# Kernel tuning notes

Hardware: AMD Instinct MI355X
Metric: run time of the kernel (lower is better)

## Reference

```python
import jax, jax.numpy as jnp
import numpy as np

EPS = 1e-6
K = 20
B, N = 4, 4096
HID, CDIM = 128, 64


def vn_lin(W, x):
    # W: [Cout, Cin], x: [B, Cin, 3, ...] -> [B, Cout, 3, ...]
    return jnp.einsum('oc,bc...->bo...', W, x)


def vn_leaky(x, d, ns=0.0):
    # vector-neuron leaky ReLU: reflect the part of x anti-aligned with direction d
    dot = jnp.sum(x * d, axis=2, keepdims=True)
    dsq = jnp.sum(d * d, axis=2, keepdims=True)
    return ns * x + (1.0 - ns) * jnp.where(dot >= 0, x, x - (dot / (dsq + EPS)) * d)


def vn_max_pool(x, Wd):
    # pool over the LAST axis, picking per-(b,c) the vector maximizing <x, d>
    d = vn_lin(Wd, x)
    dot = jnp.sum(x * d, axis=2, keepdims=True)            # [B,C,1,...,L]
    idx = jnp.broadcast_to(jnp.argmax(dot, axis=-1), x.shape[:-1])
    return jnp.take_along_axis(x, idx[..., None], axis=-1)[..., 0]


def graph_feature_cross(pts, k):
    # pts: [B, N, 3] -> [B, 3ch, 3vec, N, k] with channels (nbr-x, x, cross(nbr,x))
    sq = jnp.sum(pts * pts, axis=-1)
    inner = jnp.einsum('bnd,bmd->bnm', pts, pts)
    neg_dist = 2.0 * inner - sq[:, :, None] - sq[:, None, :]
    _, idx = jax.lax.top_k(neg_dist, k)                     # [B, N, k]
    nbr = jax.vmap(lambda p, i: p[i])(pts, idx)             # [B, N, k, 3]
    x = jnp.broadcast_to(pts[:, :, None, :], nbr.shape)
    cross = jnp.cross(nbr, x, axis=-1)
    feat = jnp.stack([nbr - x, x, cross], axis=3)           # [B, N, k, 3ch, 3vec]
    return jnp.transpose(feat, (0, 3, 4, 1, 2))


def resblock(x, a0, f0, a1, f1, sc):
    net = vn_lin(f0, vn_leaky(x, vn_lin(a0, x)))
    dx = vn_lin(f1, vn_leaky(net, vn_lin(a1, net)))
    return vn_lin(sc, x) + dx


def _init(key, shape, fan_in):
    return jax.random.normal(key, shape, jnp.float32) / np.sqrt(fan_in)


def setup_inputs():
    key = jax.random.key(0)
    ks = jax.random.split(key, 14)
    return {
        'pc': jax.random.normal(ks[0], (B, N, 3), jnp.float32),
        'conv_Wf': _init(ks[1], (64, 3), 3),
        'conv_Wd': _init(ks[2], (64, 3), 3),
        'pool_pos_Wd': _init(ks[3], (64, 64), 64),
        'fc_pos_W': _init(ks[4], (2 * HID, 64), 64),
        'blk_a0': _init(ks[5], (5, 2 * HID, 2 * HID), 2 * HID),
        'blk_f0': _init(ks[6], (5, HID, 2 * HID), 2 * HID),
        'blk_a1': _init(ks[7], (5, HID, HID), HID),
        'blk_f1': _init(ks[8], (5, HID, HID), HID),
        'blk_sc': _init(ks[9], (5, HID, 2 * HID), 2 * HID),
        'pool_Wd': _init(ks[10], (5, HID, HID), HID),
        'actc_Wd': _init(ks[11], (HID, HID), HID),
        'fcc_W': _init(ks[12], (CDIM, HID), HID),
    }


def reference(pc, conv_Wf, conv_Wd, pool_pos_Wd, fc_pos_W, blk_a0, blk_f0, blk_a1, blk_f1, blk_sc, pool_Wd, actc_Wd, fcc_W):
    b = pc.shape[0]
    feat = graph_feature_cross(pc, K)                         # [B,3,3,N,k]
    net = vn_leaky(vn_lin(conv_Wf, feat), vn_lin(conv_Wd, feat))  # [B,64,3,N,k]
    net = vn_max_pool(net, pool_pos_Wd)                       # [B,64,3,N] (pool over k)
    net = vn_lin(fc_pos_W, net)                               # [B,256,3,N]
    for i in range(5):
        net = resblock(net, blk_a0[i], blk_f0[i], blk_a1[i], blk_f1[i], blk_sc[i])  # [B,128,3,N]
        if i < 4:
            pooled = vn_max_pool(net, pool_Wd[i])             # [B,128,3] (pool over N)
            net = jnp.concatenate([net, jnp.broadcast_to(pooled[..., None], net.shape)], axis=1)
    net = vn_max_pool(net, pool_Wd[4])                        # [B,128,3]
    c = vn_lin(fcc_W, vn_leaky(net, vn_lin(actc_Wd, net)))    # [B,64,3]
    return c.reshape(b, -1)                                   # [B,192]
```

## Files before the change

### kernel.cpp

```cpp
#include <hip/hip_runtime.h>
#include <hip/hip_bf16.h>
#include <math.h>

#define NPTS 4096
#define NB 4
#define KNN 20
#define NCOLS (3*NPTS)
#define NEG_INF (-__builtin_huge_valf())
#define DNEG_INF (-__builtin_huge_val())

typedef _Float16 f16x8 __attribute__((ext_vector_type(8)));
typedef _Float16 f16x4 __attribute__((ext_vector_type(4)));
typedef float f32x4 __attribute__((ext_vector_type(4)));

#define WOFF_FC 0
#define WOFF_A0 16384
#define WOFF_F0 344064
#define WOFF_A1 507904
#define WOFF_F1 589824
#define WOFF_SC 671744
#define WOFF_PW 835584
#define WTOT    917504

__global__ __launch_bounds__(512) void knn_kernel(const float* __restrict__ pc,
                                                  int* __restrict__ idx) {
  __shared__ float pts[NPTS*3];
  __shared__ double msv[2][8];
  __shared__ int    msn[2][8];
  int b = blockIdx.x >> 10;
  int rowblk = blockIdx.x & 1023;
  const float* pb = pc + (size_t)b*NPTS*3;
  for (int i = threadIdx.x; i < NPTS*3; i += 512) pts[i] = pb[i];
  __syncthreads();
  int wave = threadIdx.x >> 6;
  int lane = threadIdx.x & 63;
  int row  = wave >> 1;
  int half = wave & 1;
  int l128 = half*64 + lane;
  int n = rowblk*4 + row;
  double pn0 = pts[n*3+0], pn1 = pts[n*3+1], pn2 = pts[n*3+2];
  double sqn = pn0*pn0 + pn1*pn1 + pn2*pn2;
  double nd[32];
#pragma unroll
  for (int j = 0; j < 32; ++j) {
    int m = j*128 + l128;
    double q0 = pts[m*3+0], q1 = pts[m*3+1], q2 = pts[m*3+2];
    double inner = pn0*q0 + pn1*q1 + pn2*q2;
    double sqm = q0*q0 + q1*q1 + q2*q2;
    nd[j] = 2.0*inner - sqn - sqm;
  }
  double gm[2]; int gj[2];
#pragma unroll
  for (int g = 0; g < 2; ++g) {
    double v = nd[g*16]; int jb = g*16;
#pragma unroll
    for (int jj = 1; jj < 16; ++jj) {
      int j = g*16 + jj;
      bool take = nd[j] > v;
      v = take ? nd[j] : v;
      jb = take ? j : jb;
    }
    gm[g] = v; gj[g] = jb;
  }
  int* orow = idx + ((size_t)b*NPTS + n)*KNN;
  for (int t = 0; t < KNN; ++t) {
    double bv = gm[0]; int bj = gj[0];
    if (gm[1] > bv) { bv = gm[1]; bj = gj[1]; }
    int bm = bj*128 + l128;
#pragma unroll
    for (int s = 1; s < 64; s <<= 1) {
      double ov = __shfl_xor(bv, s, 64);
      int om = __shfl_xor(bm, s, 64);
      bool take = (ov > bv) || (ov == bv && om < bm);
      bv = take ? ov : bv;
      bm = take ? om : bm;
    }
    if (lane == 0) { msv[t&1][wave] = bv; msn[t&1][wave] = bm; }
    __syncthreads();
    {
      double pv = msv[t&1][wave^1]; int pm = msn[t&1][wave^1];
      bool take = (pv > bv) || (pv == bv && pm < bm);
      bv = take ? pv : bv;
      bm = take ? pm : bm;
    }
    if (half == 0 && lane == 0) orow[t] = bm;
    if (t < KNN-1) {
      int vic_l128 = bm & 127;
      int jw = bm >> 7;
      int vic_half = vic_l128 >> 6;
      if (vic_half == half) {
        bool iswl = (l128 == vic_l128);
        int gw = jw >> 4;
#define REBUILD(G) { \
  _Pragma("unroll") \
  for (int jj = 0; jj < 16; ++jj) { \
    int j = (G)*16 + jj; \
    if (iswl && j == jw) nd[j] = DNEG_INF; \
  } \
  double v = nd[(G)*16]; int jb = (G)*16; \
  _Pragma("unroll") \
  for (int jj = 1; jj < 16; ++jj) { \
    int j = (G)*16 + jj; \
    bool take = nd[j] > v; \
    v = take ? nd[j] : v; \
    jb = take ? j : jb; \
  } \
  gm[G] = v; gj[G] = jb; \
}
        if (gw == 0) REBUILD(0)
        else         REBUILD(1)
#undef REBUILD
      }
    }
  }
}

#define ECH 5
__global__ __launch_bounds__(128) void edgeconv_kernel(
    const float* __restrict__ pc, const int* __restrict__ knnidx,
    const float* __restrict__ Wf, const float* __restrict__ Wd,
    const float* __restrict__ Wp, float* __restrict__ outp) {
  __shared__ float xls[2*ECH*3*64];
  int wave = threadIdx.x >> 6, lane = threadIdx.x & 63;
  int pid0 = blockIdx.x * 2;
  int b = pid0 >> 12;
  int n = (pid0 & (NPTS-1)) + wave;
  const float* pb = pc + (size_t)b*NPTS*3;
  int c = lane;
  float wrow[64];
#pragma unroll
  for (int j = 0; j < 64; ++j) wrow[j] = Wp[c*64 + j];
  float wf0 = Wf[c*3+0], wf1 = Wf[c*3+1], wf2 = Wf[c*3+2];
  float wd0 = Wd[c*3+0], wd1 = Wd[c*3+1], wd2 = Wd[c*3+2];
  float f9[9];
#pragma unroll
  for (int i = 0; i < 9; ++i) f9[i] = 0.0f;
  if (lane < KNN) {
    int j = knnidx[((size_t)b*NPTS + n)*KNN + lane];
    float q0 = pb[j*3+0], q1 = pb[j*3+1], q2 = pb[j*3+2];
    float x0 = pb[n*3+0], x1 = pb[n*3+1], x2 = pb[n*3+2];
    f9[0] = q0-x0; f9[1] = q1-x1; f9[2] = q2-x2;
    f9[3] = x0;    f9[4] = x1;    f9[5] = x2;
    f9[6] = q1*x2 - q2*x1;
    f9[7] = q2*x0 - q0*x2;
    f9[8] = q0*x1 - q1*x0;
  }
  float* xw = &xls[wave*ECH*3*64];
  double bdot = DNEG_INF;
  float bx0 = 0.f, bx1 = 0.f, bx2 = 0.f;
  for (int k0 = 0; k0 < KNN; k0 += ECH) {
    for (int kc = 0; kc < ECH; ++kc) {
      int kk = k0 + kc;
      float fch[9];
#pragma unroll
      for (int i = 0; i < 9; ++i) fch[i] = __shfl(f9[i], kk, 64);
      float fv[3], dv[3];
#pragma unroll
      for (int v = 0; v < 3; ++v) {
        fv[v] = wf0*fch[v] + wf1*fch[3+v] + wf2*fch[6+v];
        dv[v] = wd0*fch[v] + wd1*fch[3+v] + wd2*fch[6+v];
      }
      float dot = fv[0]*dv[0] + fv[1]*dv[1] + fv[2]*dv[2];
      if (dot < 0.0f) {
        float dsq = dv[0]*dv[0] + dv[1]*dv[1] + dv[2]*dv[2];
        float s = dot / (dsq + 1e-6f);
        fv[0] -= s*dv[0]; fv[1] -= s*dv[1]; fv[2] -= s*dv[2];
      }
      xw[(0*ECH+kc)*64 + c] = fv[0];
      xw[(1*ECH+kc)*64 + c] = fv[1];
      xw[(2*ECH+kc)*64 + c] = fv[2];
    }
    for (int kc = 0; kc < ECH; ++kc) {
      float a0 = 0.f, a1 = 0.f, a2 = 0.f;
#pragma unroll
      for (int j = 0; j < 64; j += 4) {
        float4 v0 = *(const float4*)&xw[(0*ECH+kc)*64 + j];
        float4 v1 = *(const float4*)&xw[(1*ECH+kc)*64 + j];
        float4 v2 = *(const float4*)&xw[(2*ECH+kc)*64 + j];
        a0 += wrow[j]*v0.x + wrow[j+1]*v0.y + wrow[j+2]*v0.z + wrow[j+3]*v0.w;
        a1 += wrow[j]*v1.x + wrow[j+1]*v1.y + wrow[j+2]*v1.z + wrow[j+3]*v1.w;
        a2 += wrow[j]*v2.x + wrow[j+1]*v2.y + wrow[j+2]*v2.z + wrow[j+3]*v2.w;
      }
      float xc0 = xw[(0*ECH+kc)*64 + c];
      float xc1 = xw[(1*ECH+kc)*64 + c];
      float xc2 = xw[(2*ECH+kc)*64 + c];
      double dd = (double)xc0*a0 + (double)xc1*a1 + (double)xc2*a2;
      bool take = dd > bdot;
      bdot = take ? dd : bdot;
      bx0 = take ? xc0 : bx0;
      bx1 = take ? xc1 : bx1;
      bx2 = take ? xc2 : bx2;
    }
  }
  outp[((size_t)b*NCOLS + 0*NPTS + n)*64 + c] = bx0;
  outp[((size_t)b*NCOLS + 1*NPTS + n)*64 + c] = bx1;
  outp[((size_t)b*NCOLS + 2*NPTS + n)*64 + c] = bx2;
}

__global__ __launch_bounds__(256) void wsplit_kernel(
    const float* __restrict__ fc, const float* __restrict__ a0,
    const float* __restrict__ f0, const float* __restrict__ a1,
    const float* __restrict__ f1, const float* __restrict__ sc,
    const float* __restrict__ pw, _Float16* __restrict__ outp) {
  int i = blockIdx.x*256 + threadIdx.x;
  const float* src; int off;
  if      (i < WOFF_A0) { src = fc; off = WOFF_FC; }
  else if (i < WOFF_F0) { src = a0; off = WOFF_A0; }
  else if (i < WOFF_A1) { src = f0; off = WOFF_F0; }
  else if (i < WOFF_F1) { src = a1; off = WOFF_A1; }
  else if (i < WOFF_SC) { src = f1; off = WOFF_F1; }
  else if (i < WOFF_PW) { src = sc; off = WOFF_SC; }
  else                  { src = pw; off = WOFF_PW; }
  float w = src[i - off];
  _Float16 h = (_Float16)w;
  outp[i] = h;
  outp[i + WTOT] = (_Float16)(w - (float)h);
}

__global__ __launch_bounds__(256) void bias2_kernel(
    const float* __restrict__ Wa0, const float* __restrict__ Wsc,
    const float* __restrict__ pooled,
    float* __restrict__ biasA, float* __restrict__ biasS) {
  int id = blockIdx.x*256 + threadIdx.x;
  const float* W; float* dst; int Cout; int idx;
  if (id < NB*3*256) { W = Wa0; dst = biasA; Cout = 256; idx = id; }
  else               { W = Wsc; dst = biasS; Cout = 128; idx = id - NB*3*256; }
  int co = idx % Cout; int t = idx / Cout;
  int v = t % 3; int b = t / 3;
  double acc = 0.0;
  const float* wr = W + (size_t)co*256 + 128;
  const float* pp = pooled + (size_t)b*384 + v;
#pragma unroll 4
  for (int c = 0; c < 128; ++c)
    acc += (double)wr[c] * (double)pp[c*3];
  dst[idx] = (float)acc;
}

#define LDP 40
__global__ __launch_bounds__(256) void gemm_mfma(
    const _Float16* __restrict__ Wh, const _Float16* __restrict__ Wl,
    const float* __restrict__ X, const float* __restrict__ Z,
    const float* __restrict__ bias, float* __restrict__ Y,
    int Cin, int Wstride, int ldX, int ldY, int ldZ, int addZ, int Cbias) {
  __shared__ __align__(16) _Float16 Ah[64*LDP];
  __shared__ __align__(16) _Float16 Al[64*LDP];
  __shared__ __align__(16) _Float16 Bh[128*LDP];
  __shared__ __align__(16) _Float16 Bl[128*LDP];
  int b = blockIdx.z;
  int sp0 = blockIdx.x * 64;
  int co0 = blockIdx.y * 128;
  const float* Xb = X + ((size_t)b*NCOLS + sp0) * ldX;
  int t = threadIdx.x;
  int arow = t >> 2, akoff = (t & 3) * 8;
  int brow = t >> 1, bkoff = (t & 1) * 16;
  int wid = t >> 6, lane = t & 63;
  int wr = (wid >> 1) * 32, wc = (wid & 1) * 64;
  int lrow = lane & 15, lk = (lane >> 4) * 8;
  f32x4 acc[2][4];
#pragma unroll
  for (int f = 0; f < 2; ++f)
#pragma unroll
    for (int g = 0; g < 4; ++g)
#pragma unroll
      for (int r = 0; r < 4; ++r) acc[f][g][r] = 0.0f;

  for (int k0 = 0; k0 < Cin; k0 += 32) {
    const float* xs = Xb + (size_t)arow*ldX + k0 + akoff;
    float xv[8];
    *(float4*)&xv[0] = *(const float4*)&xs[0];
    *(float4*)&xv[4] = *(const float4*)&xs[4];
    _Float16 xh[8], xl[8];
#pragma unroll
    for (int j = 0; j < 8; ++j) {
      _Float16 h = (_Float16)xv[j];
      xh[j] = h; xl[j] = (_Float16)(xv[j] - (float)h);
    }
    *(f16x8*)&Ah[arow*LDP + akoff] = *(f16x8*)&xh[0];
    *(f16x8*)&Al[arow*LDP + akoff] = *(f16x8*)&xl[0];
    const _Float16* whs = Wh + (size_t)(co0 + brow)*Wstride + k0 + bkoff;
    const _Float16* wls = Wl + (size_t)(co0 + brow)*Wstride + k0 + bkoff;
    *(f16x8*)&Bh[brow*LDP + bkoff]     = *(const f16x8*)&whs[0];
    *(f16x8*)&Bh[brow*LDP + bkoff + 8] = *(const f16x8*)&whs[8];
    *(f16x8*)&Bl[brow*LDP + bkoff]     = *(const f16x8*)&wls[0];
    *(f16x8*)&Bl[brow*LDP + bkoff + 8] = *(const f16x8*)&wls[8];
    __syncthreads();
    f16x8 ah[2], al[2], bh[4], bl[4];
#pragma unroll
    for (int f = 0; f < 2; ++f) {
      ah[f] = *(f16x8*)&Ah[(wr + f*16 + lrow)*LDP + lk];
      al[f] = *(f16x8*)&Al[(wr + f*16 + lrow)*LDP + lk];
    }
#pragma unroll
    for (int g = 0; g < 4; ++g) {
      bh[g] = *(f16x8*)&Bh[(wc + g*16 + lrow)*LDP + lk];
      bl[g] = *(f16x8*)&Bl[(wc + g*16 + lrow)*LDP + lk];
    }
#pragma unroll
    for (int f = 0; f < 2; ++f)
#pragma unroll
      for (int g = 0; g < 4; ++g) {
        acc[f][g] = __builtin_amdgcn_mfma_f32_16x16x32_f16(ah[f], bh[g], acc[f][g], 0, 0, 0);
        acc[f][g] = __builtin_amdgcn_mfma_f32_16x16x32_f16(ah[f], bl[g], acc[f][g], 0, 0, 0);
        acc[f][g] = __builtin_amdgcn_mfma_f32_16x16x32_f16(al[f], bh[g], acc[f][g], 0, 0, 0);
      }
    __syncthreads();
  }
  int lr0 = (lane >> 4) * 4, lc = lane & 15;
  float badd[4] = {0.f, 0.f, 0.f, 0.f};
  if (bias) {
    int v = sp0 >> 12;
    const float* brow2 = bias + ((size_t)b*3 + v)*Cbias;
#pragma unroll
    for (int g = 0; g < 4; ++g) badd[g] = brow2[co0 + wc + g*16 + lc];
  }
#pragma unroll
  for (int f = 0; f < 2; ++f)
#pragma unroll
    for (int g = 0; g < 4; ++g)
#pragma unroll
      for (int r = 0; r < 4; ++r) {
        int sp = sp0 + wr + f*16 + lr0 + r;
        int co = co0 + wc + g*16 + lc;
        float val = acc[f][g][r] + badd[g];
        if (addZ) val += Z[((size_t)b*NCOLS + sp)*ldZ + co];
        Y[((size_t)b*NCOLS + sp)*ldY + co] = val;
      }
}

__global__ __launch_bounds__(256) void gemm_dual(
    const _Float16* __restrict__ W1h, const _Float16* __restrict__ W1l,
    const _Float16* __restrict__ W2h, const _Float16* __restrict__ W2l,
    const float* __restrict__ X1, const float* __restrict__ X2s,
    const float* __restrict__ bias, float* __restrict__ Y,
    int K2, int ldY, int Cbias) {
  __shared__ __align__(16) _Float16 Ah[64*LDP];
  __shared__ __align__(16) _Float16 Al[64*LDP];
  __shared__ __align__(16) _Float16 Bh[128*LDP];
  __shared__ __align__(16) _Float16 Bl[128*LDP];
  int b = blockIdx.z;
  int sp0 = blockIdx.x * 64;
  int co0 = blockIdx.y * 128;
  int t = threadIdx.x;
  int arow = t >> 2, akoff = (t & 3) * 8;
  int brow = t >> 1, bkoff = (t & 1) * 16;
  int wid = t >> 6, lane = t & 63;
  int wr = (wid >> 1) * 32, wc = (wid & 1) * 64;
  int lrow = lane & 15, lk = (lane >> 4) * 8;
  f32x4 acc[2][4];
#pragma unroll
  for (int f = 0; f < 2; ++f)
#pragma unroll
    for (int g = 0; g < 4; ++g)
#pragma unroll
      for (int r = 0; r < 4; ++r) acc[f][g][r] = 0.0f;

  int Ktot = 128 + K2;
  for (int k0 = 0; k0 < Ktot; k0 += 32) {
    const float* xs;
    const _Float16 *whs, *wls;
    if (k0 < 128) {
      xs  = X1 + ((size_t)b*NCOLS + sp0 + arow)*128 + k0 + akoff;
      whs = W1h + (size_t)(co0 + brow)*128 + k0 + bkoff;
      wls = W1l + (size_t)(co0 + brow)*128 + k0 + bkoff;
    } else {
      xs  = X2s + ((size_t)b*NCOLS + sp0 + arow)*256 + (k0-128) + akoff;
      whs = W2h + (size_t)(co0 + brow)*256 + (k0-128) + bkoff;
      wls = W2l + (size_t)(co0 + brow)*256 + (k0-128) + bkoff;
    }
    float xv[8];
    *(float4*)&xv[0] = *(const float4*)&xs[0];
    *(float4*)&xv[4] = *(const float4*)&xs[4];
    _Float16 xh[8], xl[8];
#pragma unroll
    for (int j = 0; j < 8; ++j) {
      _Float16 h = (_Float16)xv[j];
      xh[j] = h; xl[j] = (_Float16)(xv[j] - (float)h);
    }
    *(f16x8*)&Ah[arow*LDP + akoff] = *(f16x8*)&xh[0];
    *(f16x8*)&Al[arow*LDP + akoff] = *(f16x8*)&xl[0];
    *(f16x8*)&Bh[brow*LDP + bkoff]     = *(const f16x8*)&whs[0];
    *(f16x8*)&Bh[brow*LDP + bkoff + 8] = *(const f16x8*)&whs[8];
    *(f16x8*)&Bl[brow*LDP + bkoff]     = *(const f16x8*)&wls[0];
    *(f16x8*)&Bl[brow*LDP + bkoff + 8] = *(const f16x8*)&wls[8];
    __syncthreads();
    f16x8 ah[2], al[2], bh[4], bl[4];
#pragma unroll
    for (int f = 0; f < 2; ++f) {
      ah[f] = *(f16x8*)&Ah[(wr + f*16 + lrow)*LDP + lk];
      al[f] = *(f16x8*)&Al[(wr + f*16 + lrow)*LDP + lk];
    }
#pragma unroll
    for (int g = 0; g < 4; ++g) {
      bh[g] = *(f16x8*)&Bh[(wc + g*16 + lrow)*LDP + lk];
      bl[g] = *(f16x8*)&Bl[(wc + g*16 + lrow)*LDP + lk];
    }
#pragma unroll
    for (int f = 0; f < 2; ++f)
#pragma unroll
      for (int g = 0; g < 4; ++g) {
        acc[f][g] = __builtin_amdgcn_mfma_f32_16x16x32_f16(ah[f], bh[g], acc[f][g], 0, 0, 0);
        acc[f][g] = __builtin_amdgcn_mfma_f32_16x16x32_f16(ah[f], bl[g], acc[f][g], 0, 0, 0);
        acc[f][g] = __builtin_amdgcn_mfma_f32_16x16x32_f16(al[f], bh[g], acc[f][g], 0, 0, 0);
      }
    __syncthreads();
  }
  int lr0 = (lane >> 4) * 4, lc = lane & 15;
  float badd[4] = {0.f, 0.f, 0.f, 0.f};
  if (bias) {
    int v = sp0 >> 12;
    const float* brow2 = bias + ((size_t)b*3 + v)*Cbias;
#pragma unroll
    for (int g = 0; g < 4; ++g) badd[g] = brow2[co0 + wc + g*16 + lc];
  }
#pragma unroll
  for (int f = 0; f < 2; ++f)
#pragma unroll
    for (int g = 0; g < 4; ++g)
#pragma unroll
      for (int r = 0; r < 4; ++r) {
        int sp = sp0 + wr + f*16 + lr0 + r;
        int co = co0 + wc + g*16 + lc;
        Y[((size_t)b*NCOLS + sp)*ldY + co] = acc[f][g][r] + badd[g];
      }
}

template<int FM>
__global__ __launch_bounds__(256) void gemm_leaky(
    const _Float16* __restrict__ Wh, const _Float16* __restrict__ Wl,
    const float* __restrict__ X, const float* __restrict__ pooled,
    const float* __restrict__ bias, float* __restrict__ Y,
    int Cin, int Wstride, int ldX, int ldY, int Cbias) {
  constexpr int BM = FM*32;
  __shared__ __align__(16) _Float16 Ah[BM*LDP];
  __shared__ __align__(16) _Float16 Al[BM*LDP];
  __shared__ __align__(16) _Float16 Bh[128*LDP];
  __shared__ __align__(16) _Float16 Bl[128*LDP];
  int b = blockIdx.z;
  int n0 = blockIdx.x * BM;
  int co0 = blockIdx.y * 128;
  int t = threadIdx.x;
  constexpr int APT = BM/8;
  constexpr int TPR = 32/APT;
  int arow = t / TPR, akoff = (t % TPR) * APT;
  int brow = t >> 1, bkoff = (t & 1) * 16;
  int wid = t >> 6, lane = t & 63;
  int wr = (wid >> 1) * (BM/2), wc = (wid & 1) * 64;
  int lrow = lane & 15, lk = (lane >> 4) * 8;
  f32x4 acc[3][FM][4];
#pragma unroll
  for (int v = 0; v < 3; ++v)
#pragma unroll
    for (int f = 0; f < FM; ++f)
#pragma unroll
      for (int g = 0; g < 4; ++g)
#pragma unroll
        for (int r = 0; r < 4; ++r) acc[v][f][g][r] = 0.0f;

  for (int v = 0; v < 3; ++v) {
    const float* Xb = X + ((size_t)b*NCOLS + (size_t)v*NPTS + n0) * ldX;
    for (int k0 = 0; k0 < Cin; k0 += 32) {
      const float* xs = Xb + (size_t)arow*ldX + k0 + akoff;
      float xv[APT];
#pragma unroll
      for (int j = 0; j < APT; j += 4)
        *(float4*)&xv[j] = *(const float4*)&xs[j];
      _Float16 xh[APT], xl[APT];
#pragma unroll
      for (int j = 0; j < APT; ++j) {
        _Float16 h = (_Float16)xv[j];
        xh[j] = h; xl[j] = (_Float16)(xv[j] - (float)h);
      }
      if (APT == 8) {
        *(f16x8*)&Ah[arow*LDP + akoff] = *(f16x8*)&xh[0];
        *(f16x8*)&Al[arow*LDP + akoff] = *(f16x8*)&xl[0];
      } else {
        *(f16x4*)&Ah[arow*LDP + akoff] = *(f16x4*)&xh[0];
        *(f16x4*)&Al[arow*LDP + akoff] = *(f16x4*)&xl[0];
      }
      const _Float16* whs = Wh + (size_t)(co0 + brow)*Wstride + k0 + bkoff;
      const _Float16* wls = Wl + (size_t)(co0 + brow)*Wstride + k0 + bkoff;
      *(f16x8*)&Bh[brow*LDP + bkoff]     = *(const f16x8*)&whs[0];
      *(f16x8*)&Bh[brow*LDP + bkoff + 8] = *(const f16x8*)&whs[8];
      *(f16x8*)&Bl[brow*LDP + bkoff]     = *(const f16x8*)&wls[0];
      *(f16x8*)&Bl[brow*LDP + bkoff + 8] = *(const f16x8*)&wls[8];
      __syncthreads();
      f16x8 ah[FM], al[FM], bh[4], bl[4];
#pragma unroll
      for (int f = 0; f < FM; ++f) {
        ah[f] = *(f16x8*)&Ah[(wr + f*16 + lrow)*LDP + lk];
        al[f] = *(f16x8*)&Al[(wr + f*16 + lrow)*LDP + lk];
      }
#pragma unroll
      for (int g = 0; g < 4; ++g) {
        bh[g] = *(f16x8*)&Bh[(wc + g*16 + lrow)*LDP + lk];
        bl[g] = *(f16x8*)&Bl[(wc + g*16 + lrow)*LDP + lk];
      }
#pragma unroll
      for (int f = 0; f < FM; ++f)
#pragma unroll
        for (int g = 0; g < 4; ++g) {
          acc[v][f][g] = __builtin_amdgcn_mfma_f32_16x16x32_f16(ah[f], bh[g], acc[v][f][g], 0, 0, 0);
          acc[v][f][g] = __builtin_amdgcn_mfma_f32_16x16x32_f16(ah[f], bl[g], acc[v][f][g], 0, 0, 0);
          acc[v][f][g] = __builtin_amdgcn_mfma_f32_16x16x32_f16(al[f], bh[g], acc[v][f][g], 0, 0, 0);
        }
      __syncthreads();
    }
  }
  int lr0 = (lane >> 4) * 4, lc = lane & 15;
  float badd[3][4];
#pragma unroll
  for (int v = 0; v < 3; ++v)
#pragma unroll
    for (int g = 0; g < 4; ++g) {
      badd[v][g] = bias ? bias[((size_t)b*3 + v)*Cbias + co0 + wc + g*16 + lc] : 0.0f;
    }
  bool xfromX = (pooled == nullptr) || (co0 < 128);
#pragma unroll
  for (int f = 0; f < FM; ++f)
#pragma unroll
    for (int g = 0; g < 4; ++g)
#pragma unroll
      for (int r = 0; r < 4; ++r) {
        int n = n0 + wr + f*16 + lr0 + r;
        int co = co0 + wc + g*16 + lc;
        float x0, x1, x2;
        if (xfromX) {
          x0 = X[((size_t)b*NCOLS + 0*NPTS + n)*ldX + co];
          x1 = X[((size_t)b*NCOLS + 1*NPTS + n)*ldX + co];
          x2 = X[((size_t)b*NCOLS + 2*NPTS + n)*ldX + co];
        } else {
          const float* pp = pooled + (size_t)b*384 + (co - 128)*3;
          x0 = pp[0]; x1 = pp[1]; x2 = pp[2];
        }
        float d0 = acc[0][f][g][r] + badd[0][g];
        float d1 = acc[1][f][g][r] + badd[1][g];
        float d2 = acc[2][f][g][r] + badd[2][g];
        float dot = x0*d0 + x1*d1 + x2*d2;
        float u0 = x0, u1 = x1, u2 = x2;
        if (dot < 0.0f) {
          float dsq = d0*d0 + d1*d1 + d2*d2;
          float s = dot / (dsq + 1e-6f);
          u0 = x0 - s*d0; u1 = x1 - s*d1; u2 = x2 - s*d2;
        }
        Y[((size_t)b*NCOLS + 0*NPTS + n)*ldY + co] = u0;
        Y[((size_t)b*NCOLS + 1*NPTS + n)*ldY + co] = u1;
        Y[((size_t)b*NCOLS + 2*NPTS + n)*ldY + co] = u2;
      }
}

__global__ __launch_bounds__(256) void pool1_kernel(
    const float* __restrict__ Net, const float* __restrict__ Dm,
    double* __restrict__ pv, int* __restrict__ pn, int ldN, int ldD) {
  __shared__ double sv[256];
  __shared__ int sn[256];
  int b = blockIdx.y;
  int n0 = blockIdx.x * 64;
  int c = threadIdx.x & 127;
  int half = threadIdx.x >> 7;
  double bv = DNEG_INF; int bn = 0x7fffffff;
  for (int i = 0; i < 32; ++i) {
    int n = n0 + 2*i + half;
    size_t r0 = ((size_t)b*NCOLS + n);
    double dot =
        (double)Net[(r0)*ldN + c]              * (double)Dm[(r0)*ldD + c]
      + (double)Net[(r0 + NPTS)*ldN + c]       * (double)Dm[(r0 + NPTS)*ldD + c]
      + (double)Net[(r0 + 2*NPTS)*ldN + c]     * (double)Dm[(r0 + 2*NPTS)*ldD + c];
    if (dot > bv) { bv = dot; bn = n; }
  }
  sv[threadIdx.x] = bv; sn[threadIdx.x] = bn;
  __syncthreads();
  if (half == 0) {
    double v1 = sv[threadIdx.x + 128]; int n1 = sn[threadIdx.x + 128];
    if (v1 > bv || (v1 == bv && n1 < bn)) { bv = v1; bn = n1; }
    pv[((size_t)b*64 + blockIdx.x)*128 + c] = bv;
    pn[((size_t)b*64 + blockIdx.x)*128 + c] = bn;
  }
}

__global__ __launch_bounds__(128) void pool2_kernel(
    const double* __restrict__ pv, const int* __restrict__ pn,
    const float* __restrict__ Net, float* __restrict__ pooled, int ldN) {
  int b = blockIdx.x, c = threadIdx.x;
  double bv = DNEG_INF; int bn = 0x7fffffff;
  for (int ch = 0; ch < 64; ++ch) {
    double v = pv[((size_t)b*64 + ch)*128 + c];
    int nn = pn[((size_t)b*64 + ch)*128 + c];
    if (v > bv || (v == bv && nn < bn)) { bv = v; bn = nn; }
  }
#pragma unroll
  for (int v = 0; v < 3; ++v)
    pooled[(size_t)b*384 + c*3 + v] = Net[((size_t)b*NCOLS + v*NPTS + bn)*ldN + c];
}

__global__ __launch_bounds__(128) void head_kernel(
    const float* __restrict__ pooled, const float* __restrict__ Wa,
    const float* __restrict__ Wc, float* __restrict__ out) {
  __shared__ float xp[128*3], up[128*3];
  int b = blockIdx.x, c = threadIdx.x;
#pragma unroll
  for (int v = 0; v < 3; ++v) xp[c*3+v] = pooled[(size_t)b*384 + c*3 + v];
  __syncthreads();
  float a0 = 0.f, a1 = 0.f, a2 = 0.f;
  for (int j = 0; j < 128; ++j) {
    float w = Wa[c*128+j];
    a0 += w*xp[j*3+0]; a1 += w*xp[j*3+1]; a2 += w*xp[j*3+2];
  }
  float x0 = xp[c*3+0], x1 = xp[c*3+1], x2 = xp[c*3+2];
  float dot = x0*a0 + x1*a1 + x2*a2;
  float u0 = x0, u1 = x1, u2 = x2;
  if (dot < 0.0f) {
    float dsq = a0*a0 + a1*a1 + a2*a2;
    float s = dot / (dsq + 1e-6f);
    u0 = x0 - s*a0; u1 = x1 - s*a1; u2 = x2 - s*a2;
  }
  up[c*3+0] = u0; up[c*3+1] = u1; up[c*3+2] = u2;
  __syncthreads();
  if (c < 64) {
    float o0 = 0.f, o1 = 0.f, o2 = 0.f;
    for (int j = 0; j < 128; ++j) {
      float w = Wc[c*128+j];
      o0 += w*up[j*3+0]; o1 += w*up[j*3+1]; o2 += w*up[j*3+2];
    }
    out[(size_t)b*192 + c*3 + 0] = o0;
    out[(size_t)b*192 + c*3 + 1] = o1;
    out[(size_t)b*192 + c*3 + 2] = o2;
  }
}

extern "C" void kernel_launch(void* const* d_in, const int* in_sizes, int n_in,
                              void* d_out, int out_size, void* d_ws, size_t ws_size,
                              hipStream_t stream) {
  const float* pc    = (const float*)d_in[0];
  const float* cWf   = (const float*)d_in[1];
  const float* cWd   = (const float*)d_in[2];
  const float* pposW = (const float*)d_in[3];
  const float* fcW   = (const float*)d_in[4];
  const float* ba0   = (const float*)d_in[5];
  const float* bf0   = (const float*)d_in[6];
  const float* ba1   = (const float*)d_in[7];
  const float* bf1   = (const float*)d_in[8];
  const float* bscW  = (const float*)d_in[9];
  const float* pWd   = (const float*)d_in[10];
  const float* aWd   = (const float*)d_in[11];
  const float* fccW  = (const float*)d_in[12];
  float* out = (float*)d_out;
  char* ws = (char*)d_ws;
  const size_t MB = 1u << 20;
  const size_t KB = 1u << 10;
  int*      idxb   = (int*)(ws);
  float*    X1     = (float*)(ws + 2*MB);
  float*    X2     = (float*)(ws + 52*MB);
  float*    conv   = (float*)(ws + 52*MB);
  float*    T      = (float*)(ws + 102*MB);
  float*    T2     = T;
  float*    Hn     = (float*)(ws + 152*MB);
  float*    pooled = (float*)(ws + 178*MB);
  double*   pv     = (double*)(ws + 178*MB + 16*KB);
  int*      pn     = (int*)(ws + 178*MB + 288*KB);
  float*    biasA  = (float*)(ws + 178*MB + 448*KB);
  float*    biasS  = (float*)(ws + 178*MB + 512*KB);
  _Float16* Wsp    = (_Float16*)(ws + 179*MB);
  _Float16* WspLo  = Wsp + WTOT;

  wsplit_kernel<<<WTOT/256, 256, 0, stream>>>(fcW, ba0, bf0, ba1, bf1, bscW, pWd, Wsp);
  knn_kernel<<<NB*NPTS/4, 512, 0, stream>>>(pc, idxb);
  edgeconv_kernel<<<NB*NPTS/2, 128, 0, stream>>>(pc, idxb, cWf, cWd, pposW, conv);
  gemm_mfma<<<dim3(192, 2, NB), 256, 0, stream>>>(Wsp + WOFF_FC, WspLo + WOFF_FC,
      conv, nullptr, nullptr, X1, 64, 64, 64, 256, 0, 0, 0);

  float* Xin = X1; float* Xout = X2;
  for (int i = 0; i < 5; ++i) {
    const _Float16* a0h = Wsp   + WOFF_A0 + (size_t)i*65536;
    const _Float16* a0l = WspLo + WOFF_A0 + (size_t)i*65536;
    const _Float16* f0h = Wsp   + WOFF_F0 + (size_t)i*32768;
    const _Float16* f0l = WspLo + WOFF_F0 + (size_t)i*32768;
    const _Float16* a1h = Wsp   + WOFF_A1 + (size_t)i*16384;
    const _Float16* a1l = WspLo + WOFF_A1 + (size_t)i*16384;
    const _Float16* f1h = Wsp   + WOFF_F1 + (size_t)i*16384;
    const _Float16* f1l = WspLo + WOFF_F1 + (size_t)i*16384;
    const _Float16* sch = Wsp   + WOFF_SC + (size_t)i*32768;
    const _Float16* scl = WspLo + WOFF_SC + (size_t)i*32768;
    const _Float16* pwh = Wsp   + WOFF_PW + (size_t)i*16384;
    const _Float16* pwl = WspLo + WOFF_PW + (size_t)i*16384;
    int KA = (i == 0) ? 256 : 128;
    const float* bA = (i == 0) ? nullptr : biasA;
    const float* bS = (i == 0) ? nullptr : biasS;
    const float* lp = (i == 0) ? nullptr : pooled;
    if (i > 0) {
      bias2_kernel<<<(NB*3*384+255)/256,256,0,stream>>>(
          ba0 + (size_t)i*65536, bscW + (size_t)i*32768, pooled, biasA, biasS);
    }
    gemm_leaky<2><<<dim3(NPTS/64, 2, NB), 256, 0, stream>>>(a0h, a0l, Xin, lp, bA, T,
        KA, 256, 256, 256, 256);
    gemm_mfma<<<dim3(192,1,NB),256,0,stream>>>(f0h, f0l, T, nullptr, nullptr, Hn,
        256, 256, 256, 128, 0, 0, 0);
    gemm_leaky<1><<<dim3(NPTS/32, 1, NB), 256, 0, stream>>>(a1h, a1l, Hn, nullptr, nullptr, T2,
        128, 128, 128, 128, 0);
    gemm_dual<<<dim3(192,1,NB),256,0,stream>>>(f1h, f1l, sch, scl, T2, Xin, bS, Xout,
        KA, 256, 128);
    gemm_mfma<<<dim3(192,1,NB),256,0,stream>>>(pwh, pwl, Xout, nullptr, nullptr, Hn,
        128, 128, 256, 128, 0, 0, 0);
    pool1_kernel<<<dim3(64,NB),256,0,stream>>>(Xout, Hn, pv, pn, 256, 128);
    pool2_kernel<<<NB,128,0,stream>>>(pv, pn, Xout, pooled, 256);
    if (i < 4) { float* tmp = Xin; Xin = Xout; Xout = tmp; }
  }
  head_kernel<<<NB,128,0,stream>>>(pooled, aWd, fccW, out);
}
```

Before: 1.340 ms.

## Fuse pool direction GEMM with per-block argmax partial pooling

```diff
diff --git a/kernel.cpp b/kernel.cpp
--- a/kernel.cpp
+++ b/kernel.cpp
@@ -548,30 +548,127 @@
       }
 }
 
-__global__ __launch_bounds__(256) void pool1_kernel(
-    const float* __restrict__ Net, const float* __restrict__ Dm,
-    double* __restrict__ pv, int* __restrict__ pn, int ldN, int ldD) {
-  __shared__ double sv[256];
-  __shared__ int sn[256];
-  int b = blockIdx.y;
+__global__ __launch_bounds__(256) void gemm_pool(
+    const _Float16* __restrict__ Wh, const _Float16* __restrict__ Wl,
+    const float* __restrict__ X,
+    double* __restrict__ pv, int* __restrict__ pn) {
+  __shared__ __align__(16) _Float16 Ah[64*LDP];
+  __shared__ __align__(16) _Float16 Al[64*LDP];
+  __shared__ __align__(16) _Float16 Bh[128*LDP];
+  __shared__ __align__(16) _Float16 Bl[128*LDP];
+  int b = blockIdx.z;
   int n0 = blockIdx.x * 64;
-  int c = threadIdx.x & 127;
-  int half = threadIdx.x >> 7;
-  double bv = DNEG_INF; int bn = 0x7fffffff;
-  for (int i = 0; i < 32; ++i) {
-    int n = n0 + 2*i + half;
-    size_t r0 = ((size_t)b*NCOLS + n);
-    double dot =
-        (double)Net[(r0)*ldN + c]              * (double)Dm[(r0)*ldD + c]
-      + (double)Net[(r0 + NPTS)*ldN + c]       * (double)Dm[(r0 + NPTS)*ldD + c]
-      + (double)Net[(r0 + 2*NPTS)*ldN + c]     * (double)Dm[(r0 + 2*NPTS)*ldD + c];
-    if (dot > bv) { bv = dot; bn = n; }
-  }
-  sv[threadIdx.x] = bv; sn[threadIdx.x] = bn;
+  int t = threadIdx.x;
+  int arow = t >> 2, akoff = (t & 3) * 8;
+  int brow = t >> 1, bkoff = (t & 1) * 16;
+  int wid = t >> 6, lane = t & 63;
+  int wr = (wid >> 1) * 32, wc = (wid & 1) * 64;
+  int lrow = lane & 15, lk = (lane >> 4) * 8;
+  f32x4 acc[3][2][4];
+#pragma unroll
+  for (int v = 0; v < 3; ++v)
+#pragma unroll
+    for (int f = 0; f < 2; ++f)
+#pragma unroll
+      for (int g = 0; g < 4; ++g)
+#pragma unroll
+        for (int r = 0; r < 4; ++r) acc[v][f][g][r] = 0.0f;
+
+  for (int v = 0; v < 3; ++v) {
+    const float* Xb = X + ((size_t)b*NCOLS + (size_t)v*NPTS + n0) * 256;
+    for (int k0 = 0; k0 < 128; k0 += 32) {
+      const float* xs = Xb + (size_t)arow*256 + k0 + akoff;
+      float xv[8];
+      *(float4*)&xv[0] = *(const float4*)&xs[0];
+      *(float4*)&xv[4] = *(const float4*)&xs[4];
+      _Float16 xh[8], xl[8];
+#pragma unroll
+      for (int j = 0; j < 8; ++j) {
+        _Float16 h = (_Float16)xv[j];
+        xh[j] = h; xl[j] = (_Float16)(xv[j] - (float)h);
+      }
+      *(f16x8*)&Ah[arow*LDP + akoff] = *(f16x8*)&xh[0];
+      *(f16x8*)&Al[arow*LDP + akoff] = *(f16x8*)&xl[0];
+      const _Float16* whs = Wh + (size_t)brow*128 + k0 + bkoff;
+      const _Float16* wls = Wl + (size_t)brow*128 + k0 + bkoff;
+      *(f16x8*)&Bh[brow*LDP + bkoff]     = *(const f16x8*)&whs[0];
+      *(f16x8*)&Bh[brow*LDP + bkoff + 8] = *(const f16x8*)&whs[8];
+      *(f16x8*)&Bl[brow*LDP + bkoff]     = *(const f16x8*)&wls[0];
+      *(f16x8*)&Bl[brow*LDP + bkoff + 8] = *(const f16x8*)&wls[8];
+      __syncthreads();
+      f16x8 ah[2], al[2], bh[4], bl[4];
+#pragma unroll
+      for (int f = 0; f < 2; ++f) {
+        ah[f] = *(f16x8*)&Ah[(wr + f*16 + lrow)*LDP + lk];
+        al[f] = *(f16x8*)&Al[(wr + f*16 + lrow)*LDP + lk];
+      }
+#pragma unroll
+      for (int g = 0; g < 4; ++g) {
+        bh[g] = *(f16x8*)&Bh[(wc + g*16 + lrow)*LDP + lk];
+        bl[g] = *(f16x8*)&Bl[(wc + g*16 + lrow)*LDP + lk];
+      }
+#pragma unroll
+      for (int f = 0; f < 2; ++f)
+#pragma unroll
+        for (int g = 0; g < 4; ++g) {
+          acc[v][f][g] = __builtin_amdgcn_mfma_f32_16x16x32_f16(ah[f], bh[g], acc[v][f][g], 0, 0, 0);
+          acc[v][f][g] = __builtin_amdgcn_mfma_f32_16x16x32_f16(ah[f], bl[g], acc[v][f][g], 0, 0, 0);
+          acc[v][f][g] = __builtin_amdgcn_mfma_f32_16x16x32_f16(al[f], bh[g], acc[v][f][g], 0, 0, 0);
+        }
+      __syncthreads();
+    }
+  }
+  int lr0 = (lane >> 4) * 4, lc = lane & 15;
+  double bestv[4]; int bestn[4];
+#pragma unroll
+  for (int g = 0; g < 4; ++g) { bestv[g] = DNEG_INF; bestn[g] = 0x7fffffff; }
+#pragma unroll
+  for (int f = 0; f < 2; ++f)
+#pragma unroll
+    for (int r = 0; r < 4; ++r) {
+      int n = n0 + wr + f*16 + lr0 + r;
+#pragma unroll
+      for (int g = 0; g < 4; ++g) {
+        int co = wc + g*16 + lc;
+        double dot =
+            (double)X[((size_t)b*NCOLS + 0*NPTS + n)*256 + co] * (double)acc[0][f][g][r]
+          + (double)X[((size_t)b*NCOLS + 1*NPTS + n)*256 + co] * (double)acc[1][f][g][r]
+          + (double)X[((size_t)b*NCOLS + 2*NPTS + n)*256 + co] * (double)acc[2][f][g][r];
+        bool take = (dot > bestv[g]) || (dot == bestv[g] && n < bestn[g]);
+        bestv[g] = take ? dot : bestv[g];
+        bestn[g] = take ? n : bestn[g];
+      }
+    }
+#pragma unroll
+  for (int s = 16; s < 64; s <<= 1) {
+#pragma unroll
+    for (int g = 0; g < 4; ++g) {
+      double ov = __shfl_xor(bestv[g], s, 64);
+      int on = __shfl_xor(bestn[g], s, 64);
+      bool take = (ov > bestv[g]) || (ov == bestv[g] && on < bestn[g]);
+      bestv[g] = take ? ov : bestv[g];
+      bestn[g] = take ? on : bestn[g];
+    }
+  }
+  double* cdv = (double*)Ah;
+  int*    cdn = (int*)Bh;
+  if (lane < 16) {
+#pragma unroll
+    for (int g = 0; g < 4; ++g) {
+      cdv[(wid*4 + g)*16 + lane] = bestv[g];
+      cdn[(wid*4 + g)*16 + lane] = bestn[g];
+    }
+  }
   __syncthreads();
-  if (half == 0) {
-    double v1 = sv[threadIdx.x + 128]; int n1 = sn[threadIdx.x + 128];
-    if (v1 > bv || (v1 == bv && n1 < bn)) { bv = v1; bn = n1; }
+  if (t < 128) {
+    int c = t;
+    int wq = c >> 6;
+    int g = (c >> 4) & 3, l2 = c & 15;
+    double v0 = cdv[((wq)*4 + g)*16 + l2];   int n0v = cdn[((wq)*4 + g)*16 + l2];
+    double v1 = cdv[((wq+2)*4 + g)*16 + l2]; int n1v = cdn[((wq+2)*4 + g)*16 + l2];
+    bool take = (v1 > v0) || (v1 == v0 && n1v < n0v);
+    double bv = take ? v1 : v0;
+    int bn = take ? n1v : n0v;
     pv[((size_t)b*64 + blockIdx.x)*128 + c] = bv;
     pn[((size_t)b*64 + blockIdx.x)*128 + c] = bn;
   }
@@ -674,10 +771,10 @@
     const _Float16* a0l = WspLo + WOFF_A0 + (size_t)i*65536;
     const _Float16* f0h = Wsp   + WOFF_F0 + (size_t)i*32768;
     const _Float16* f0l = WspLo + WOFF_F0 + (size_t)i*32768;
+    const _Float16* f1h = Wsp   + WOFF_F1 + (size_t)i*16384;
+    const _Float16* f1l = WspLo + WOFF_F1 + (size_t)i*16384;
     const _Float16* a1h = Wsp   + WOFF_A1 + (size_t)i*16384;
     const _Float16* a1l = WspLo + WOFF_A1 + (size_t)i*16384;
-    const _Float16* f1h = Wsp   + WOFF_F1 + (size_t)i*16384;
-    const _Float16* f1l = WspLo + WOFF_F1 + (size_t)i*16384;
     const _Float16* sch = Wsp   + WOFF_SC + (size_t)i*32768;
     const _Float16* scl = WspLo + WOFF_SC + (size_t)i*32768;
     const _Float16* pwh = Wsp   + WOFF_PW + (size_t)i*16384;
@@ -698,9 +795,7 @@
         128, 128, 128, 128, 0);
     gemm_dual<<<dim3(192,1,NB),256,0,stream>>>(f1h, f1l, sch, scl, T2, Xin, bS, Xout,
         KA, 256, 128);
-    gemm_mfma<<<dim3(192,1,NB),256,0,stream>>>(pwh, pwl, Xout, nullptr, nullptr, Hn,
-        128, 128, 256, 128, 0, 0, 0);
-    pool1_kernel<<<dim3(64,NB),256,0,stream>>>(Xout, Hn, pv, pn, 256, 128);
+    gemm_pool<<<dim3(NPTS/64,1,NB),256,0,stream>>>(pwh, pwl, Xout, pv, pn);
     pool2_kernel<<<NB,128,0,stream>>>(pv, pn, Xout, pooled, 256);
     if (i < 4) { float* tmp = Xin; Xin = Xout; Xout = tmp; }
   }
```

Result: faster. 1.310 ms (-2.3%).
